# Kernel tuning notes

Measured on AMD Instinct MI355X. Metric: run time of the kernel, lower is better.

Reference implementation:

```python
import jax, jax.numpy as jnp
import numpy as np

B = 16384   # model_batches: parallel chaos-game chains
T = 512     # num_points: sequential IFS iterations per chain
N = 16      # num_matrices: affine functions in the IFS code


def setup_inputs() -> dict:
    key = jax.random.key(0)
    k1, k2, k3, k4, k5 = jax.random.split(key, 5)
    # uniform_sample1d(min=-5, max=5, dim=(B, 2))
    init_points = jax.random.uniform(k1, (B, 2), dtype=jnp.float32, minval=-5.0, maxval=5.0)
    # contractive affine maps: scale so spectral norm < 1 (ContractiveFunction)
    weights = jax.random.normal(k2, (N, 2, 2), dtype=jnp.float32) * 0.35
    biases = jax.random.normal(k3, (N, 2), dtype=jnp.float32) * 0.5
    opacities = jax.random.uniform(k4, (N,), dtype=jnp.float32)
    # fractal_code: precomputed per-step, per-chain function index (randomize_sequence=True)
    code = jax.random.randint(k5, (T, B), 0, N, dtype=jnp.int32)
    return {"init_points": init_points, "weights": weights, "biases": biases,
            "opacities": opacities, "code": code}


def reference(init_points, weights, biases, opacities, code):
    # ParallelIFS.forward: sequential chaos-game recurrence with gathered params.
    def step(p, idx):  # p: (B,2), idx: (B,) int
        W = weights[idx]            # (B,2,2) gather
        b = biases[idx]             # (B,2)
        p = jnp.einsum('bij,bj->bi', W, p) + b
        op = opacities[idx][:, None]  # (B,1)
        return p, jnp.concatenate([p, op], axis=1)  # emit (x, y, opacity)

    _, pts = jax.lax.scan(step, init_points, code)   # (T, B, 3)
    pts = pts.reshape(-1, 3)                          # (T*B, 3)
    ops = pts[:, 2:3]
    # apply_mv_transform: fixed model-view affine, world [-1,1] -> screen [0,1]
    tpoints = pts[:, :2] * 0.5 + 0.5
    top_points = jnp.concatenate([tpoints, ops], axis=1)
    return top_points
```

## Files before the change

### kernel.cpp

```cpp
#include <hip/hip_runtime.h>


#define B_PTS 16384
#define T_STEPS 512
#define N_TR 16
#define PTS_PER_BLK 64
#define WAVES 16
#define L_CHUNK 32
#define THREADS 1024

__global__ __launch_bounds__(THREADS, 1)
void ifs_scan_kernel(const float* __restrict__ init_pts,
                     const float* __restrict__ weights,
                     const float* __restrict__ biases,
                     const float* __restrict__ opac,
                     const int*   __restrict__ code,
                     float*       __restrict__ out)
{
    __shared__ unsigned char codeL[T_STEPS][PTS_PER_BLK];
    __shared__ float4 tabA[N_TR];
    __shared__ float4 tabB[N_TR];
    __shared__ float4 mapsA[WAVES][PTS_PER_BLK];
    __shared__ float2 mapsB[WAVES][PTS_PER_BLK];

    const int tid  = threadIdx.x;
    const int lane = tid & 63;
    const int wv   = tid >> 6;
    const int base = blockIdx.x * PTS_PER_BLK;

    if (tid < N_TR) {
        const int n = tid;
        tabA[n] = make_float4(weights[n*4+0], weights[n*4+1],
                              weights[n*4+2], weights[n*4+3]);
        tabB[n] = make_float4(biases[n*2+0], biases[n*2+1], opac[n], 0.f);
    }

    #pragma unroll
    for (int i = 0; i < 8; ++i) {
        const int j  = tid + i * THREADS;
        const int t  = j >> 4;
        const int p4 = (j & 15) << 2;
        const int4 v = *reinterpret_cast<const int4*>(&code[(size_t)t * B_PTS + base + p4]);
        uchar4 pk;
        pk.x = (unsigned char)v.x; pk.y = (unsigned char)v.y;
        pk.z = (unsigned char)v.z; pk.w = (unsigned char)v.w;
        *reinterpret_cast<uchar4*>(&codeL[t][p4]) = pk;
    }
    __syncthreads();

    float m00 = 1.f, m01 = 0.f, m10 = 0.f, m11 = 1.f, vx = 0.f, vy = 0.f;
    const int t0 = wv * L_CHUNK;
    #pragma unroll 8
    for (int s = 0; s < L_CHUNK; ++s) {
        const int idx = codeL[t0 + s][lane];
        const float4 A  = tabA[idx];
        const float4 Bv = tabB[idx];
        const float n00 = A.x * m00 + A.y * m10;
        const float n01 = A.x * m01 + A.y * m11;
        const float n10 = A.z * m00 + A.w * m10;
        const float n11 = A.z * m01 + A.w * m11;
        const float nvx = A.x * vx + A.y * vy + Bv.x;
        const float nvy = A.z * vx + A.w * vy + Bv.y;
        m00 = n00; m01 = n01; m10 = n10; m11 = n11; vx = nvx; vy = nvy;
    }
    mapsA[wv][lane] = make_float4(m00, m01, m10, m11);
    mapsB[wv][lane] = make_float2(vx, vy);
    __syncthreads();

    float px = init_pts[(size_t)(base + lane) * 2 + 0];
    float py = init_pts[(size_t)(base + lane) * 2 + 1];
    for (int c = 0; c < wv; ++c) {
        const float4 M = mapsA[c][lane];
        const float2 V = mapsB[c][lane];
        const float nx = M.x * px + M.y * py + V.x;
        const float ny = M.z * px + M.w * py + V.y;
        px = nx; py = ny;
    }

    float* op = out + (size_t)((size_t)t0 * B_PTS + base + lane) * 3;
    #pragma unroll 8
    for (int s = 0; s < L_CHUNK; ++s) {
        const int idx = codeL[t0 + s][lane];
        const float4 A  = tabA[idx];
        const float4 Bv = tabB[idx];
        const float nx = A.x * px + A.y * py + Bv.x;
        const float ny = A.z * px + A.w * py + Bv.y;
        px = nx; py = ny;
        op[0] = px * 0.5f + 0.5f;
        op[1] = py * 0.5f + 0.5f;
        op[2] = Bv.z;
        op += (size_t)B_PTS * 3;
    }
}

extern "C" void kernel_launch(void* const* d_in, const int* in_sizes, int n_in,
                              void* d_out, int out_size, void* d_ws, size_t ws_size,
                              hipStream_t stream) {
    const float* init_pts = (const float*)d_in[0];
    const float* weights  = (const float*)d_in[1];
    const float* biases   = (const float*)d_in[2];
    const float* opac     = (const float*)d_in[3];
    const int*   code     = (const int*)d_in[4];
    float*       out      = (float*)d_out;

    ifs_scan_kernel<<<B_PTS / PTS_PER_BLK, THREADS, 0, stream>>>(
        init_pts, weights, biases, opac, code, out);
}
```

Measured before the change: 140.2 us.

## Replace chunked parallel scan with single-pass sequential chains and code prefetch

Drops the two-phase time-chunked scan (composing affine maps per chunk, then replaying) and instead runs each chain sequentially in one 64-thread block, prefetching the next 16 code indices into registers ahead of use. This removes the redundant matrix composition work, the large LDS code staging and the block-wide syncs. In exchange it gives up most of the thread-level parallelism: only one wave per block runs a 512-step dependent loop, so latency hiding relies on register prefetch and outstanding stores.

```diff
diff --git a/kernel.cpp b/kernel.cpp
--- a/kernel.cpp
+++ b/kernel.cpp
@@ -4,92 +4,84 @@
 #define B_PTS 16384
 #define T_STEPS 512
 #define N_TR 16
-#define PTS_PER_BLK 64
-#define WAVES 16
-#define L_CHUNK 32
-#define THREADS 1024
+#define GRP 8
 
-__global__ __launch_bounds__(THREADS, 1)
-void ifs_scan_kernel(const float* __restrict__ init_pts,
+__global__ __launch_bounds__(64, 1)
+void ifs_single_pass(const float* __restrict__ init_pts,
                      const float* __restrict__ weights,
                      const float* __restrict__ biases,
                      const float* __restrict__ opac,
                      const int*   __restrict__ code,
                      float*       __restrict__ out)
 {
-    __shared__ unsigned char codeL[T_STEPS][PTS_PER_BLK];
     __shared__ float4 tabA[N_TR];
     __shared__ float4 tabB[N_TR];
-    __shared__ float4 mapsA[WAVES][PTS_PER_BLK];
-    __shared__ float2 mapsB[WAVES][PTS_PER_BLK];
 
-    const int tid  = threadIdx.x;
-    const int lane = tid & 63;
-    const int wv   = tid >> 6;
-    const int base = blockIdx.x * PTS_PER_BLK;
+    const int lane = threadIdx.x;
+    const int b    = blockIdx.x * 64 + lane;
 
-    if (tid < N_TR) {
-        const int n = tid;
-        tabA[n] = make_float4(weights[n*4+0], weights[n*4+1],
-                              weights[n*4+2], weights[n*4+3]);
-        tabB[n] = make_float4(biases[n*2+0], biases[n*2+1], opac[n], 0.f);
-    }
-
-    #pragma unroll
-    for (int i = 0; i < 8; ++i) {
-        const int j  = tid + i * THREADS;
-        const int t  = j >> 4;
-        const int p4 = (j & 15) << 2;
-        const int4 v = *reinterpret_cast<const int4*>(&code[(size_t)t * B_PTS + base + p4]);
-        uchar4 pk;
-        pk.x = (unsigned char)v.x; pk.y = (unsigned char)v.y;
-        pk.z = (unsigned char)v.z; pk.w = (unsigned char)v.w;
-        *reinterpret_cast<uchar4*>(&codeL[t][p4]) = pk;
+    if (lane < N_TR) {
+        tabA[lane] = make_float4(weights[lane*4+0], weights[lane*4+1],
+                                 weights[lane*4+2], weights[lane*4+3]);
+        tabB[lane] = make_float4(biases[lane*2+0], biases[lane*2+1],
+                                 opac[lane], 0.f);
     }
     __syncthreads();
 
-    float m00 = 1.f, m01 = 0.f, m10 = 0.f, m11 = 1.f, vx = 0.f, vy = 0.f;
-    const int t0 = wv * L_CHUNK;
-    #pragma unroll 8
-    for (int s = 0; s < L_CHUNK; ++s) {
-        const int idx = codeL[t0 + s][lane];
-        const float4 A  = tabA[idx];
-        const float4 Bv = tabB[idx];
-        const float n00 = A.x * m00 + A.y * m10;
-        const float n01 = A.x * m01 + A.y * m11;
-        const float n10 = A.z * m00 + A.w * m10;
-        const float n11 = A.z * m01 + A.w * m11;
-        const float nvx = A.x * vx + A.y * vy + Bv.x;
-        const float nvy = A.z * vx + A.w * vy + Bv.y;
-        m00 = n00; m01 = n01; m10 = n10; m11 = n11; vx = nvx; vy = nvy;
-    }
-    mapsA[wv][lane] = make_float4(m00, m01, m10, m11);
-    mapsB[wv][lane] = make_float2(vx, vy);
-    __syncthreads();
+    const float2 p0 = *reinterpret_cast<const float2*>(&init_pts[(size_t)b * 2]);
+    float px = p0.x, py = p0.y;
 
-    float px = init_pts[(size_t)(base + lane) * 2 + 0];
-    float py = init_pts[(size_t)(base + lane) * 2 + 1];
-    for (int c = 0; c < wv; ++c) {
-        const float4 M = mapsA[c][lane];
-        const float2 V = mapsB[c][lane];
-        const float nx = M.x * px + M.y * py + V.x;
-        const float ny = M.z * px + M.w * py + V.y;
-        px = nx; py = ny;
-    }
+    int c0[GRP], c1[GRP];
+    #pragma unroll
+    for (int g = 0; g < GRP; ++g) c0[g] = code[(size_t)g * B_PTS + b];
+    #pragma unroll
+    for (int g = 0; g < GRP; ++g) c1[g] = code[(size_t)(GRP + g) * B_PTS + b];
 
-    float* op = out + (size_t)((size_t)t0 * B_PTS + base + lane) * 3;
-    #pragma unroll 8
-    for (int s = 0; s < L_CHUNK; ++s) {
-        const int idx = codeL[t0 + s][lane];
-        const float4 A  = tabA[idx];
-        const float4 Bv = tabB[idx];
-        const float nx = A.x * px + A.y * py + Bv.x;
-        const float ny = A.z * px + A.w * py + Bv.y;
-        px = nx; py = ny;
-        op[0] = px * 0.5f + 0.5f;
-        op[1] = py * 0.5f + 0.5f;
-        op[2] = Bv.z;
-        op += (size_t)B_PTS * 3;
+    float* op = out + (size_t)b * 3;
+    const size_t step_stride = (size_t)B_PTS * 3;
+
+    for (int t0 = 0; t0 < T_STEPS; t0 += 2 * GRP) {
+        int n0[GRP], n1[GRP];
+        #pragma unroll
+        for (int g = 0; g < GRP; ++g) {
+            const int tl = t0 + 2 * GRP + g;
+            n0[g] = code[(size_t)(tl < T_STEPS ? tl : T_STEPS - 1) * B_PTS + b];
+        }
+        #pragma unroll
+        for (int g = 0; g < GRP; ++g) {
+            const int tl = t0 + 3 * GRP + g;
+            n1[g] = code[(size_t)(tl < T_STEPS ? tl : T_STEPS - 1) * B_PTS + b];
+        }
+
+        #pragma unroll
+        for (int g = 0; g < GRP; ++g) {
+            const int idx   = c0[g];
+            const float4 A  = tabA[idx];
+            const float4 Bv = tabB[idx];
+            const float nx = fmaf(A.x, px, fmaf(A.y, py, Bv.x));
+            const float ny = fmaf(A.z, px, fmaf(A.w, py, Bv.y));
+            px = nx; py = ny;
+            op[0] = fmaf(px, 0.5f, 0.5f);
+            op[1] = fmaf(py, 0.5f, 0.5f);
+            op[2] = Bv.z;
+            op += step_stride;
+        }
+        #pragma unroll
+        for (int g = 0; g < GRP; ++g) {
+            const int idx   = c1[g];
+            const float4 A  = tabA[idx];
+            const float4 Bv = tabB[idx];
+            const float nx = fmaf(A.x, px, fmaf(A.y, py, Bv.x));
+            const float ny = fmaf(A.z, px, fmaf(A.w, py, Bv.y));
+            px = nx; py = ny;
+            op[0] = fmaf(px, 0.5f, 0.5f);
+            op[1] = fmaf(py, 0.5f, 0.5f);
+            op[2] = Bv.z;
+            op += step_stride;
+        }
+
+        #pragma unroll
+        for (int g = 0; g < GRP; ++g) { c0[g] = n0[g]; c1[g] = n1[g]; }
     }
 }
 
@@ -103,6 +95,6 @@
     const int*   code     = (const int*)d_in[4];
     float*       out      = (float*)d_out;
 
-    ifs_scan_kernel<<<B_PTS / PTS_PER_BLK, THREADS, 0, stream>>>(
+    ifs_single_pass<<<B_PTS / 64, 64, 0, stream>>>(
         init_pts, weights, biases, opac, code, out);
 }
```

Measured after the change: 157.4 us. 1.12x slower.

## Precompute pairwise composed maps and keep per-chain codes in registers

Applied to the files above, without the earlier changes.

Builds a 256-entry shared table of composed affine maps for every ordered pair of transforms, so the chunk-composition phase does half as many dependent steps. Code indices are now loaded straight from global into a 32-entry register array per thread, replacing the staging pass into a shared byte array. The output loop uses explicit fmaf. The risks are higher register pressure and the extra setup work to build the pair table.

```diff
diff --git a/kernel.cpp b/kernel.cpp
--- a/kernel.cpp
+++ b/kernel.cpp
@@ -8,18 +8,20 @@
 #define WAVES 16
 #define L_CHUNK 32
 #define THREADS 1024
+#define NPAIR 256
 
 __global__ __launch_bounds__(THREADS, 1)
-void ifs_scan_kernel(const float* __restrict__ init_pts,
-                     const float* __restrict__ weights,
-                     const float* __restrict__ biases,
-                     const float* __restrict__ opac,
-                     const int*   __restrict__ code,
-                     float*       __restrict__ out)
+void ifs_scan_v2(const float* __restrict__ init_pts,
+                 const float* __restrict__ weights,
+                 const float* __restrict__ biases,
+                 const float* __restrict__ opac,
+                 const int*   __restrict__ code,
+                 float*       __restrict__ out)
 {
-    __shared__ unsigned char codeL[T_STEPS][PTS_PER_BLK];
     __shared__ float4 tabA[N_TR];
     __shared__ float4 tabB[N_TR];
+    __shared__ float4 pairA[NPAIR];
+    __shared__ float2 pairB[NPAIR];
     __shared__ float4 mapsA[WAVES][PTS_PER_BLK];
     __shared__ float2 mapsB[WAVES][PTS_PER_BLK];
 
@@ -27,67 +29,74 @@
     const int lane = tid & 63;
     const int wv   = tid >> 6;
     const int base = blockIdx.x * PTS_PER_BLK;
+    const int b    = base + lane;
+    const int t0   = wv * L_CHUNK;
+
+    int c[L_CHUNK];
+    #pragma unroll
+    for (int s = 0; s < L_CHUNK; ++s)
+        c[s] = code[(size_t)(t0 + s) * B_PTS + b];
 
     if (tid < N_TR) {
-        const int n = tid;
-        tabA[n] = make_float4(weights[n*4+0], weights[n*4+1],
-                              weights[n*4+2], weights[n*4+3]);
-        tabB[n] = make_float4(biases[n*2+0], biases[n*2+1], opac[n], 0.f);
+        tabA[tid] = make_float4(weights[tid*4+0], weights[tid*4+1],
+                                weights[tid*4+2], weights[tid*4+3]);
+        tabB[tid] = make_float4(biases[tid*2+0], biases[tid*2+1], opac[tid], 0.f);
     }
-
-    #pragma unroll
-    for (int i = 0; i < 8; ++i) {
-        const int j  = tid + i * THREADS;
-        const int t  = j >> 4;
-        const int p4 = (j & 15) << 2;
-        const int4 v = *reinterpret_cast<const int4*>(&code[(size_t)t * B_PTS + base + p4]);
-        uchar4 pk;
-        pk.x = (unsigned char)v.x; pk.y = (unsigned char)v.y;
-        pk.z = (unsigned char)v.z; pk.w = (unsigned char)v.w;
-        *reinterpret_cast<uchar4*>(&codeL[t][p4]) = pk;
+    if (tid >= 64 && tid < 64 + NPAIR) {
+        const int n = tid - 64;
+        const int i = n & 15, j = n >> 4;
+        const float ai = weights[i*4+0], bi = weights[i*4+1];
+        const float ci = weights[i*4+2], di = weights[i*4+3];
+        const float aj = weights[j*4+0], bj = weights[j*4+1];
+        const float cj = weights[j*4+2], dj = weights[j*4+3];
+        const float bxi = biases[i*2+0], byi = biases[i*2+1];
+        const float bxj = biases[j*2+0], byj = biases[j*2+1];
+        pairA[n] = make_float4(aj*ai + bj*ci, aj*bi + bj*di,
+                               cj*ai + dj*ci, cj*bi + dj*di);
+        pairB[n] = make_float2(aj*bxi + bj*byi + bxj,
+                               cj*bxi + dj*byi + byj);
     }
     __syncthreads();
 
     float m00 = 1.f, m01 = 0.f, m10 = 0.f, m11 = 1.f, vx = 0.f, vy = 0.f;
-    const int t0 = wv * L_CHUNK;
-    #pragma unroll 8
-    for (int s = 0; s < L_CHUNK; ++s) {
-        const int idx = codeL[t0 + s][lane];
-        const float4 A  = tabA[idx];
-        const float4 Bv = tabB[idx];
-        const float n00 = A.x * m00 + A.y * m10;
-        const float n01 = A.x * m01 + A.y * m11;
-        const float n10 = A.z * m00 + A.w * m10;
-        const float n11 = A.z * m01 + A.w * m11;
-        const float nvx = A.x * vx + A.y * vy + Bv.x;
-        const float nvy = A.z * vx + A.w * vy + Bv.y;
+    #pragma unroll
+    for (int k = 0; k < L_CHUNK / 2; ++k) {
+        const int pidx = (c[2*k+1] << 4) | c[2*k];
+        const float4 P = pairA[pidx];
+        const float2 V = pairB[pidx];
+        const float n00 = P.x * m00 + P.y * m10;
+        const float n01 = P.x * m01 + P.y * m11;
+        const float n10 = P.z * m00 + P.w * m10;
+        const float n11 = P.z * m01 + P.w * m11;
+        const float nvx = P.x * vx + P.y * vy + V.x;
+        const float nvy = P.z * vx + P.w * vy + V.y;
         m00 = n00; m01 = n01; m10 = n10; m11 = n11; vx = nvx; vy = nvy;
     }
     mapsA[wv][lane] = make_float4(m00, m01, m10, m11);
     mapsB[wv][lane] = make_float2(vx, vy);
     __syncthreads();
 
-    float px = init_pts[(size_t)(base + lane) * 2 + 0];
-    float py = init_pts[(size_t)(base + lane) * 2 + 1];
-    for (int c = 0; c < wv; ++c) {
-        const float4 M = mapsA[c][lane];
-        const float2 V = mapsB[c][lane];
+    const float2 p0 = *reinterpret_cast<const float2*>(&init_pts[(size_t)b * 2]);
+    float px = p0.x, py = p0.y;
+    for (int q = 0; q < wv; ++q) {
+        const float4 M = mapsA[q][lane];
+        const float2 V = mapsB[q][lane];
         const float nx = M.x * px + M.y * py + V.x;
         const float ny = M.z * px + M.w * py + V.y;
         px = nx; py = ny;
     }
 
-    float* op = out + (size_t)((size_t)t0 * B_PTS + base + lane) * 3;
+    float* op = out + (size_t)((size_t)t0 * B_PTS + b) * 3;
     #pragma unroll 8
     for (int s = 0; s < L_CHUNK; ++s) {
-        const int idx = codeL[t0 + s][lane];
+        const int idx   = c[s];
         const float4 A  = tabA[idx];
         const float4 Bv = tabB[idx];
-        const float nx = A.x * px + A.y * py + Bv.x;
-        const float ny = A.z * px + A.w * py + Bv.y;
+        const float nx = fmaf(A.x, px, fmaf(A.y, py, Bv.x));
+        const float ny = fmaf(A.z, px, fmaf(A.w, py, Bv.y));
         px = nx; py = ny;
-        op[0] = px * 0.5f + 0.5f;
-        op[1] = py * 0.5f + 0.5f;
+        op[0] = fmaf(px, 0.5f, 0.5f);
+        op[1] = fmaf(py, 0.5f, 0.5f);
         op[2] = Bv.z;
         op += (size_t)B_PTS * 3;
     }
@@ -103,6 +112,6 @@
     const int*   code     = (const int*)d_in[4];
     float*       out      = (float*)d_out;
 
-    ifs_scan_kernel<<<B_PTS / PTS_PER_BLK, THREADS, 0, stream>>>(
+    ifs_scan_v2<<<B_PTS / PTS_PER_BLK, THREADS, 0, stream>>>(
         init_pts, weights, biases, opac, code, out);
 }
```

New measurement: 139.1 us. No clear change (-0.8%).
